# Kernel tuning notes

Hardware: AMD Instinct MI355X
Metric: run time of the kernel (lower is better)

Reference implementation:

```python
import jax, jax.numpy as jnp
import numpy as np

B, M, D, E, K, T = 8192, 6, 128, 5, 2, 60
SHARED_W, UNSHARED_W, LB_W = 0.3, 0.7, 0.01

def _gelu(x):
    return jax.nn.gelu(x, approximate=False)

def _mlp3(x, w1, b1, w2, b2, w3, b3):
    h = _gelu(x @ w1 + b1)
    h = _gelu(h @ w2 + b2)
    return h @ w3 + b3

def _expert_stack(x, w1, b1, w2, b2, w3, b3):
    # x: [N, D]; weights stacked over experts e -> grouped GEMMs
    h = _gelu(jnp.einsum('nd,edh->enh', x, w1) + b1[:, None, :])
    h = _gelu(jnp.einsum('enh,ehg->eng', h, w2) + b2[:, None, :])
    return jnp.einsum('eng,ego->eno', h, w3) + b3[:, None, :]

def setup_inputs():
    key = jax.random.key(0)
    ks = iter(jax.random.split(key, 64))
    p = lambda shape, s=0.05: s * jax.random.normal(next(ks), shape, dtype=jnp.float32)
    return {
        'mode_features': jax.random.normal(next(ks), (B, M, D), dtype=jnp.float32),
        'rw1': p((D, 256)), 'rb1': p((256,)), 'rw2': p((256, 128)), 'rb2': p((128,)),
        'rw3': p((128, E)), 'rb3': p((E,)),
        'sh_tw1': p((D, 256)), 'sh_tb1': p((256,)), 'sh_tw2': p((256, 256)), 'sh_tb2': p((256,)),
        'sh_tw3': p((256, T * 2)), 'sh_tb3': p((T * 2,)),
        'sh_sw1': p((D, 128)), 'sh_sb1': p((128,)), 'sh_sw2': p((128, 64)), 'sh_sb2': p((64,)),
        'sh_sw3': p((64, 1)), 'sh_sb3': p((1,)),
        'ex_tw1': p((E, D, 256)), 'ex_tb1': p((E, 256)), 'ex_tw2': p((E, 256, 256)), 'ex_tb2': p((E, 256)),
        'ex_tw3': p((E, 256, T * 2)), 'ex_tb3': p((E, T * 2)),
        'ex_sw1': p((E, D, 128)), 'ex_sb1': p((E, 128)), 'ex_sw2': p((E, 128, 64)), 'ex_sb2': p((E, 64)),
        'ex_sw3': p((E, 64, 1)), 'ex_sb3': p((E, 1)),
    }

def reference(mode_features, rw1, rb1, rw2, rb2, rw3, rb3,
              sh_tw1, sh_tb1, sh_tw2, sh_tb2, sh_tw3, sh_tb3,
              sh_sw1, sh_sb1, sh_sw2, sh_sb2, sh_sw3, sh_sb3,
              ex_tw1, ex_tb1, ex_tw2, ex_tb2, ex_tw3, ex_tb3,
              ex_sw1, ex_sb1, ex_sw2, ex_sb2, ex_sw3, ex_sb3):
    b, m, d = mode_features.shape
    x = mode_features.reshape(b * m, d)
    # router (Dropout is identity in eval mode)
    logits = _mlp3(x, rw1, rb1, rw2, rb2, rw3, rb3)                 # [N, E]
    probs = jax.nn.softmax(logits, axis=-1)
    router_logits = logits.reshape(b, m, E)
    topk_logits, topk_idx = jax.lax.top_k(router_logits, K)         # [B, M, K]
    topk_probs = jax.nn.softmax(topk_logits, axis=-1)
    # shared expert on all tokens
    shared_traj = _mlp3(x, sh_tw1, sh_tb1, sh_tw2, sh_tb2, sh_tw3, sh_tb3).reshape(b, m, T, 2)
    shared_score = _mlp3(x, sh_sw1, sh_sb1, sh_sw2, sh_sb2, sh_sw3, sh_sb3).reshape(b, m)
    # all unshared experts computed densely (torch code also computes these for expert_predictions)
    traj_all = _expert_stack(x, ex_tw1, ex_tb1, ex_tw2, ex_tb2, ex_tw3, ex_tb3).reshape(E, b, m, T, 2)
    score_all = _expert_stack(x, ex_sw1, ex_sb1, ex_sw2, ex_sb2, ex_sw3, ex_sb3).reshape(E, b, m)
    # top-k combine: gather selected expert outputs (same math as the torch dispatch + index_add_)
    traj_bme = jnp.transpose(traj_all, (1, 2, 0, 3, 4))             # [B, M, E, T, 2]
    score_bme = jnp.transpose(score_all, (1, 2, 0))                 # [B, M, E]
    idx5 = jnp.broadcast_to(topk_idx[..., None, None], (b, m, K, T, 2))
    sel_traj = jnp.take_along_axis(traj_bme, idx5, axis=2)          # [B, M, K, T, 2]
    sel_score = jnp.take_along_axis(score_bme, topk_idx, axis=2)    # [B, M, K]
    unshared_traj = jnp.einsum('bmktc,bmk->bmtc', sel_traj, topk_probs)
    unshared_score = jnp.sum(sel_score * topk_probs, axis=-1)
    final_traj = SHARED_W * shared_traj + UNSHARED_W * unshared_traj
    final_score = SHARED_W * shared_score + UNSHARED_W * unshared_score
    # load-balance aux loss
    avg_probs = jnp.mean(probs, axis=0)                             # [E]
    entropy = -jnp.sum(avg_probs * jnp.log(avg_probs + 1e-8))
    l2 = jnp.mean((avg_probs - 1.0 / E) ** 2)
    aux_loss = -entropy * LB_W + 0.01 * l2
    return (final_traj, final_score, router_logits, topk_idx, aux_loss, traj_all, score_all)
```

## Files before the change

kernel.cpp:

```cpp
#include <hip/hip_runtime.h>
#include <hip/hip_bf16.h>
#include <cstdint>
#include <cstddef>

static constexpr int N_TOK = 49152;
static constexpr size_t OFF_TRAJ     = 0;
static constexpr size_t OFF_SCORE    = 5898240;
static constexpr size_t OFF_LOGITS   = 5947392;
static constexpr size_t OFF_IDX      = 6193152;
static constexpr size_t OFF_AUX      = 6291456;
static constexpr size_t OFF_TRAJALL  = 6291457;
static constexpr size_t OFF_SCOREALL = 35782657;

typedef short s16x8 __attribute__((ext_vector_type(8)));
typedef float f32x4 __attribute__((ext_vector_type(4)));
typedef f32x4 f32x4u __attribute__((aligned(4)));
typedef unsigned int u32;
typedef unsigned short u16;

static constexpr u32 O_T1 = 0,      O_T2 = 196608, O_T3 = 589824;
static constexpr u32 O_S1 = 774144, O_S2 = 872448;
static constexpr u32 OB_T1 = 0, OB_T2 = 1536, OB_T3 = 3072, OB_S1 = 3792, OB_S2 = 4560;
static constexpr u32 OW_S3 = 4944, OB_S3 = 5328;

__device__ __forceinline__ float gelu_exact(float x) {
    return 0.5f * x * (1.0f + erff(x * 0.70710678118654752440f));
}
__device__ __forceinline__ float gelu_f(float x) {
    const float x2 = x * x;
    const float u  = x * fmaf(0.07135486172f, x2, 1.5957691216057308f);
    const float t  = __expf(-u);
    return x * __builtin_amdgcn_rcpf(1.0f + t);
}
__device__ __forceinline__ float bf2f(u16 u) {
    return __uint_as_float(((u32)u) << 16);
}
__device__ __forceinline__ u16 f2bf(float v) {
    return ((__hip_bfloat16_raw)__float2bfloat16(v)).x;
}
__device__ __forceinline__ void gload16(const u16* g, u16* l) {
    __builtin_amdgcn_global_load_lds(
        (const __attribute__((address_space(1))) u32*)g,
        (__attribute__((address_space(3))) u32*)l, 16, 0, 0);
}
#define MFMA16(a, b, c) __builtin_amdgcn_mfma_f32_16x16x32_bf16(a, b, c, 0, 0, 0)
#define SBAR() __builtin_amdgcn_sched_barrier(0)

__device__ __forceinline__ s16x8 lds_frag(const u16* buf, int RBu16, int r, int c) {
    return *(const s16x8*)&buf[r * RBu16 + ((c ^ (r & 7)) << 3)];
}
__device__ __forceinline__ void lds_store4(u16* buf, int RBu16, int r, int colb,
                                           float v0, float v1, float v2, float v3) {
    const int ch = (colb >> 3) ^ (r & 7);
    ushort4 st = { f2bf(v0), f2bf(v1), f2bf(v2), f2bf(v3) };
    *(ushort4*)&buf[r * RBu16 + ch * 8 + (colb & 7)] = st;
}

__global__ __launch_bounds__(512, 2)
void router_fused(const float* __restrict__ x, const float* __restrict__ rw1,
                  const float* __restrict__ rb1, const float* __restrict__ rw2,
                  const float* __restrict__ rb2, const float* __restrict__ rw3,
                  const float* __restrict__ rb3, u16* __restrict__ xb,
                  float* __restrict__ logits, float* __restrict__ oidx,
                  float* __restrict__ tp, int* __restrict__ ti,
                  float* __restrict__ part)
{
    __shared__ float bufA[32 * 128];
    __shared__ float bufB[32 * 256];
    __shared__ float bufC[32 * 256];

    const int tid  = threadIdx.x;
    const int row0 = blockIdx.x * 32;
    const int tg   = tid >> 6;
    const int cl   = tid & 63;
    const int t0   = tg * 4;

    {
        const float* src = x + (size_t)row0 * 128;
        #pragma unroll
        for (int i = 0; i < 2; ++i)
            *(float4*)&bufA[i * 2048 + tid * 4] = *(const float4*)&src[i * 2048 + tid * 4];
    }
    __syncthreads();

    {
        u16* dst = xb + (size_t)row0 * 128;
        const int base = tid * 8;
        ushort4 o0, o1;
        o0.x = f2bf(bufA[base + 0]); o0.y = f2bf(bufA[base + 1]);
        o0.z = f2bf(bufA[base + 2]); o0.w = f2bf(bufA[base + 3]);
        o1.x = f2bf(bufA[base + 4]); o1.y = f2bf(bufA[base + 5]);
        o1.z = f2bf(bufA[base + 6]); o1.w = f2bf(bufA[base + 7]);
        *(ushort4*)&dst[base]     = o0;
        *(ushort4*)&dst[base + 4] = o1;
    }

    float acc1[4][4] = {};
    for (int k0 = 0; k0 < 128; k0 += 32) {
        __syncthreads();
        #pragma unroll
        for (int i = 0; i < 4; ++i)
            *(float4*)&bufB[i * 2048 + tid * 4] =
                *(const float4*)&rw1[(size_t)k0 * 256 + i * 2048 + tid * 4];
        __syncthreads();
        #pragma unroll
        for (int kk = 0; kk < 32; ++kk) {
            const float4 wv = *(const float4*)&bufB[kk * 256 + cl * 4];
            #pragma unroll
            for (int i = 0; i < 4; ++i) {
                const float xv = bufA[(t0 + i) * 128 + k0 + kk];
                acc1[i][0] = fmaf(xv, wv.x, acc1[i][0]);
                acc1[i][1] = fmaf(xv, wv.y, acc1[i][1]);
                acc1[i][2] = fmaf(xv, wv.z, acc1[i][2]);
                acc1[i][3] = fmaf(xv, wv.w, acc1[i][3]);
            }
        }
    }
    {
        const float4 b1 = *(const float4*)&rb1[cl * 4];
        #pragma unroll
        for (int i = 0; i < 4; ++i) {
            bufC[(t0 + i) * 256 + cl * 4 + 0] = gelu_exact(acc1[i][0] + b1.x);
            bufC[(t0 + i) * 256 + cl * 4 + 1] = gelu_exact(acc1[i][1] + b1.y);
            bufC[(t0 + i) * 256 + cl * 4 + 2] = gelu_exact(acc1[i][2] + b1.z);
            bufC[(t0 + i) * 256 + cl * 4 + 3] = gelu_exact(acc1[i][3] + b1.w);
        }
    }
    __syncthreads();

    float acc2[4][2] = {};
    for (int k0 = 0; k0 < 256; k0 += 32) {
        __syncthreads();
        #pragma unroll
        for (int i = 0; i < 2; ++i)
            *(float4*)&bufA[i * 2048 + tid * 4] =
                *(const float4*)&rw2[(size_t)k0 * 128 + i * 2048 + tid * 4];
        __syncthreads();
        #pragma unroll
        for (int kk = 0; kk < 32; ++kk) {
            const float2 wv = *(const float2*)&bufA[kk * 128 + cl * 2];
            #pragma unroll
            for (int i = 0; i < 4; ++i) {
                const float hv = bufC[(t0 + i) * 256 + k0 + kk];
                acc2[i][0] = fmaf(hv, wv.x, acc2[i][0]);
                acc2[i][1] = fmaf(hv, wv.y, acc2[i][1]);
            }
        }
    }
    {
        const float2 b2 = *(const float2*)&rb2[cl * 2];
        #pragma unroll
        for (int i = 0; i < 4; ++i) {
            bufB[(t0 + i) * 128 + cl * 2 + 0] = gelu_exact(acc2[i][0] + b2.x);
            bufB[(t0 + i) * 128 + cl * 2 + 1] = gelu_exact(acc2[i][1] + b2.y);
        }
    }
    __syncthreads();

    {
        const int tok = tid >> 4;
        const int ln  = tid & 15;
        float l5[5] = {0.f, 0.f, 0.f, 0.f, 0.f};
        #pragma unroll
        for (int kk = 0; kk < 8; ++kk) {
            const float hv = bufB[tok * 128 + ln * 8 + kk];
            #pragma unroll
            for (int e = 0; e < 5; ++e)
                l5[e] = fmaf(hv, rw3[(size_t)(ln * 8 + kk) * 5 + e], l5[e]);
        }
        #pragma unroll
        for (int off = 8; off > 0; off >>= 1)
            #pragma unroll
            for (int e = 0; e < 5; ++e)
                l5[e] += __shfl_xor(l5[e], off);

        if (ln == 0) {
            const int n = row0 + tok;
            float l[5];
            #pragma unroll
            for (int e = 0; e < 5; ++e) {
                l[e] = l5[e] + rb3[e];
                logits[(size_t)n * 5 + e] = l[e];
            }
            float m = l[0];
            #pragma unroll
            for (int e = 1; e < 5; ++e) m = fmaxf(m, l[e]);
            float p[5], s = 0.f;
            #pragma unroll
            for (int e = 0; e < 5; ++e) { p[e] = expf(l[e] - m); s += p[e]; }
            const float inv = 1.0f / s;
            #pragma unroll
            for (int e = 0; e < 5; ++e) bufC[tok * 5 + e] = p[e] * inv;

            int i0 = 0; float v0 = l[0];
            #pragma unroll
            for (int e = 1; e < 5; ++e) if (l[e] > v0) { v0 = l[e]; i0 = e; }
            int i1 = -1; float v1 = -1e30f;
            #pragma unroll
            for (int e = 0; e < 5; ++e) if (e != i0 && l[e] > v1) { v1 = l[e]; i1 = e; }

            const float t  = expf(v1 - v0);
            const float q0 = 1.0f / (1.0f + t);
            const float q1 = t / (1.0f + t);

            oidx[(size_t)n * 2]     = (float)i0;
            oidx[(size_t)n * 2 + 1] = (float)i1;
            tp[n * 2] = q0; tp[n * 2 + 1] = q1;
            ti[n * 2] = i0; ti[n * 2 + 1] = i1;
        }
    }
    __syncthreads();
    if (tid < 5) {
        float s = 0.f;
        #pragma unroll 8
        for (int t = 0; t < 32; ++t) s += bufC[t * 5 + tid];
        part[blockIdx.x * 5 + tid] = s;
    }
}

__global__ __launch_bounds__(256)
void aux_kernel(const float* __restrict__ part, float* __restrict__ aux)
{
    __shared__ float avg[5];
    const int tid = threadIdx.x;
    if (tid < 5) {
        float s = 0.f;
        for (int b = 0; b < 1536; ++b) s += part[b * 5 + tid];
        avg[tid] = s / (float)N_TOK;
    }
    __syncthreads();
    if (tid == 0) {
        float ent = 0.f, l2 = 0.f;
        #pragma unroll
        for (int e = 0; e < 5; ++e) {
            ent -= avg[e] * logf(avg[e] + 1e-8f);
            float d = avg[e] - 0.2f;
            l2 += d * d;
        }
        l2 *= (1.0f / 5.0f);
        aux[0] = -ent * 0.01f + 0.01f * l2;
    }
}

__global__ __launch_bounds__(512, 2)
void expert_fused(const u16* __restrict__ xb, const u16* __restrict__ wtb,
                  const float* __restrict__ biasp, float* __restrict__ out,
                  float* __restrict__ shtraj, float* __restrict__ shscore)
{
    __shared__ u16 xs[64 * 128];
    __shared__ u16 hb[64 * 256];
    float* hbf = (float*)hb;
    u16* s1p = hb;
    u16* s2p = hb + 64 * 128;

    const int tid  = threadIdx.x;
    const int lane = tid & 63;
    const int wave = tid >> 6;
    const int row0 = blockIdx.x * 64;
    const int e    = blockIdx.y;
    const int frow = lane & 15;
    const int kgrp = lane >> 4;
    const int c0   = wave * 32;

    #pragma unroll
    for (int i = 0; i < 2; ++i) {
        const int idx = i * 512 + tid;
        const int r = idx >> 4, c = idx & 15;
        gload16(xb + (size_t)(row0 + r) * 128 + ((c ^ (r & 7)) << 3), &xs[idx * 8]);
    }

    const int col3 = wave * 16 + kgrp * 4;
    const int r3   = (wave * 16 + frow) < 120 ? (wave * 16 + frow) : 119;

    s16x8 wf1[4][2];
    {
        const u16* w1p = wtb + O_T1 + e * 32768;
        #pragma unroll
        for (int n = 0; n < 2; ++n) {
            const u16* p = w1p + (size_t)(c0 + n * 16 + frow) * 128 + kgrp * 8;
            #pragma unroll
            for (int ks = 0; ks < 4; ++ks) wf1[ks][n] = *(const s16x8*)(p + ks * 32);
        }
    }
    SBAR();

    __syncthreads();

    f32x4 acc1[4][2] = {};
    #pragma unroll
    for (int ks = 0; ks < 4; ++ks)
        #pragma unroll
        for (int m = 0; m < 4; ++m) {
            const s16x8 a = lds_frag(xs, 128, m * 16 + frow, ks * 4 + kgrp);
            #pragma unroll
            for (int n = 0; n < 2; ++n)
                acc1[m][n] = MFMA16(wf1[ks][n], a, acc1[m][n]);
        }

    const u16* w2p = wtb + O_T2 + e * 65536;
    s16x8 wf2a[4][2];
    f32x4 bb1[2];
    #pragma unroll
    for (int n = 0; n < 2; ++n) {
        const u16* p = w2p + (size_t)(c0 + n * 16 + frow) * 256 + kgrp * 8;
        #pragma unroll
        for (int ks = 0; ks < 4; ++ks) wf2a[ks][n] = *(const s16x8*)(p + ks * 32);
        bb1[n] = *(const f32x4*)&biasp[OB_T1 + e * 256 + c0 + n * 16 + kgrp * 4];
    }
    SBAR();

    {
        #pragma unroll
        for (int n = 0; n < 2; ++n) {
            const int colb = c0 + n * 16 + kgrp * 4;
            #pragma unroll
            for (int m = 0; m < 4; ++m)
                lds_store4(hb, 256, m * 16 + frow, colb,
                           gelu_f(acc1[m][n][0] + bb1[n][0]),
                           gelu_f(acc1[m][n][1] + bb1[n][1]),
                           gelu_f(acc1[m][n][2] + bb1[n][2]),
                           gelu_f(acc1[m][n][3] + bb1[n][3]));
        }
    }
    __syncthreads();

    s16x8 wf2b[4][2];
    #pragma unroll
    for (int n = 0; n < 2; ++n) {
        const u16* p = w2p + (size_t)(c0 + n * 16 + frow) * 256 + 128 + kgrp * 8;
        #pragma unroll
        for (int ks = 0; ks < 4; ++ks) wf2b[ks][n] = *(const s16x8*)(p + ks * 32);
    }
    SBAR();

    f32x4 acc2[4][2] = {};
    #pragma unroll
    for (int ks = 0; ks < 4; ++ks)
        #pragma unroll
        for (int m = 0; m < 4; ++m) {
            const s16x8 a = lds_frag(hb, 256, m * 16 + frow, ks * 4 + kgrp);
            #pragma unroll
            for (int n = 0; n < 2; ++n)
                acc2[m][n] = MFMA16(wf2a[ks][n], a, acc2[m][n]);
        }
    #pragma unroll
    for (int ks = 0; ks < 4; ++ks)
        #pragma unroll
        for (int m = 0; m < 4; ++m) {
            const s16x8 a = lds_frag(hb, 256, m * 16 + frow, (ks + 4) * 4 + kgrp);
            #pragma unroll
            for (int n = 0; n < 2; ++n)
                acc2[m][n] = MFMA16(wf2b[ks][n], a, acc2[m][n]);
        }

    s16x8 wf3[8];
    f32x4 bb2[2];
    {
        const u16* w3p = wtb + O_T3 + e * 30720 + (size_t)r3 * 256 + kgrp * 8;
        #pragma unroll
        for (int ks = 0; ks < 8; ++ks) wf3[ks] = *(const s16x8*)(w3p + ks * 32);
        #pragma unroll
        for (int n = 0; n < 2; ++n)
            bb2[n] = *(const f32x4*)&biasp[OB_T2 + e * 256 + c0 + n * 16 + kgrp * 4];
    }
    SBAR();
    __syncthreads();

    {
        #pragma unroll
        for (int n = 0; n < 2; ++n) {
            const int colb = c0 + n * 16 + kgrp * 4;
            #pragma unroll
            for (int m = 0; m < 4; ++m)
                lds_store4(hb, 256, m * 16 + frow, colb,
                           gelu_f(acc2[m][n][0] + bb2[n][0]),
                           gelu_f(acc2[m][n][1] + bb2[n][1]),
                           gelu_f(acc2[m][n][2] + bb2[n][2]),
                           gelu_f(acc2[m][n][3] + bb2[n][3]));
        }
    }
    __syncthreads();

    s16x8 wfs1[4];
    f32x4 bb3 = *(const f32x4u*)&biasp[OB_T3 + e * 120 + (col3 < 120 ? col3 : 116)];
    {
        const u16* p = wtb + O_S1 + e * 16384 + (size_t)(wave * 16 + frow) * 128 + kgrp * 8;
        #pragma unroll
        for (int ks = 0; ks < 4; ++ks) wfs1[ks] = *(const s16x8*)(p + ks * 32);
    }
    SBAR();

    f32x4 acc3[4] = {};
    #pragma unroll
    for (int ks = 0; ks < 8; ++ks)
        #pragma unroll
        for (int m = 0; m < 4; ++m) {
            const s16x8 a = lds_frag(hb, 256, m * 16 + frow, ks * 4 + kgrp);
            acc3[m] = MFMA16(wf3[ks], a, acc3[m]);
        }
    __syncthreads();

    f32x4 accs1[4] = {};
    #pragma unroll
    for (int ks = 0; ks < 4; ++ks)
        #pragma unroll
        for (int m = 0; m < 4; ++m) {
            const s16x8 a = lds_frag(xs, 128, m * 16 + frow, ks * 4 + kgrp);
            accs1[m] = MFMA16(wfs1[ks], a, accs1[m]);
        }
    s16x8 wfs2[4];
    f32x4 bbs1;
    {
        const u16* p = wtb + O_S2 + e * 8192 + (size_t)((wave & 3) * 16 + frow) * 128 + kgrp * 8;
        #pragma unroll
        for (int ks = 0; ks < 4; ++ks) wfs2[ks] = *(const s16x8*)(p + ks * 32);
        bbs1 = *(const f32x4*)&biasp[OB_S1 + e * 128 + wave * 16 + kgrp * 4];
    }
    SBAR();
    {
        const int colb = wave * 16 + kgrp * 4;
        #pragma unroll
        for (int m = 0; m < 4; ++m)
            lds_store4(s1p, 128, m * 16 + frow, colb,
                       gelu_f(accs1[m][0] + bbs1[0]),
                       gelu_f(accs1[m][1] + bbs1[1]),
                       gelu_f(accs1[m][2] + bbs1[2]),
                       gelu_f(accs1[m][3] + bbs1[3]));
    }
    __syncthreads();

    if (wave < 4) {
        f32x4 accs2[4] = {};
        #pragma unroll
        for (int ks = 0; ks < 4; ++ks)
            #pragma unroll
            for (int m = 0; m < 4; ++m) {
                const s16x8 a = lds_frag(s1p, 128, m * 16 + frow, ks * 4 + kgrp);
                accs2[m] = MFMA16(wfs2[ks], a, accs2[m]);
            }
        const int colb = wave * 16 + kgrp * 4;
        const f32x4 bb = *(const f32x4*)&biasp[OB_S2 + e * 64 + colb];
        #pragma unroll
        for (int m = 0; m < 4; ++m)
            lds_store4(s2p, 64, m * 16 + frow, colb,
                       gelu_f(accs2[m][0] + bb[0]),
                       gelu_f(accs2[m][1] + bb[1]),
                       gelu_f(accs2[m][2] + bb[2]),
                       gelu_f(accs2[m][3] + bb[3]));
    }
    __syncthreads();

    {
        const int tok = tid >> 3;
        const int kc  = tid & 7;
        const float* w3s = biasp + OW_S3 + e * 64 + kc * 8;
        const s16x8 v = lds_frag(s2p, 64, tok, kc);
        float p = 0.f;
        #pragma unroll
        for (int j = 0; j < 8; ++j) p = fmaf(bf2f((u16)v[j]), w3s[j], p);
        p += __shfl_xor(p, 1);
        p += __shfl_xor(p, 2);
        p += __shfl_xor(p, 4);
        if (kc == 0) {
            const float val = p + biasp[OB_S3 + e];
            if (e < 5) out[OFF_SCOREALL + (size_t)e * N_TOK + row0 + tok] = val;
            else       shscore[row0 + tok] = val;
        }
    }
    __syncthreads();

    if (col3 < 120) {
        #pragma unroll
        for (int m = 0; m < 4; ++m) {
            f32x4 v;
            #pragma unroll
            for (int j = 0; j < 4; ++j) v[j] = acc3[m][j] + bb3[j];
            *(f32x4*)&hbf[(m * 16 + frow) * 124 + col3] = v;
        }
    }
    __syncthreads();

    {
        float* dst = (e < 5) ? out + OFF_TRAJALL + ((size_t)e * N_TOK + row0) * 120
                             : shtraj + (size_t)row0 * 120;
        const int head = (int)((16 - (((size_t)dst) & 15)) & 15) >> 2;
        const int nvec = (7680 - head) >> 2;
        const int tail = 7680 - head - (nvec << 2);
        if (tid < head) {
            const int t0i = tid;
            dst[t0i] = hbf[(t0i / 120) * 124 + (t0i % 120)];
        }
        if (tid >= 8 && tid < 8 + tail) {
            const int t0i = 7680 - tail + (tid - 8);
            dst[t0i] = hbf[(t0i / 120) * 124 + (t0i % 120)];
        }
        #pragma unroll
        for (int i = 0; i < 4; ++i) {
            const int v = i * 512 + tid;
            if (v < nvec) {
                const int q = head + v * 4;
                const int tok = q / 120;
                const int colq = q - tok * 120;
                f32x4 val;
                #pragma unroll
                for (int j = 0; j < 4; ++j) {
                    const int qq = q + j;
                    const int tk = qq / 120;
                    val[j] = hbf[tk * 124 + (qq - tk * 120)];
                }
                (void)tok; (void)colq;
                *(f32x4*)(dst + q) = val;
            }
        }
    }
}

__global__ __launch_bounds__(256)
void combine_all(const float* __restrict__ trajall, const float* __restrict__ shtraj,
                 const float* __restrict__ scoreall, const float* __restrict__ shscore,
                 const float* __restrict__ tp, const int* __restrict__ ti,
                 float* __restrict__ ftraj, float* __restrict__ fscore)
{
    const int i4 = blockIdx.x * 256 + threadIdx.x;
    const int n  = i4 / 30;
    const int q4 = (i4 - n * 30) * 4;
    const int i0 = ti[n * 2], i1 = ti[n * 2 + 1];
    const float p0 = tp[n * 2], p1 = tp[n * 2 + 1];

    const f32x4 a = *(const f32x4u*)&trajall[((size_t)i0 * N_TOK + n) * 120 + q4];
    const f32x4 b = *(const f32x4u*)&trajall[((size_t)i1 * N_TOK + n) * 120 + q4];
    const f32x4 s = *(const f32x4*)&shtraj[(size_t)n * 120 + q4];
    f32x4 r;
    #pragma unroll
    for (int j = 0; j < 4; ++j)
        r[j] = 0.3f * s[j] + 0.7f * (p0 * a[j] + p1 * b[j]);
    *(f32x4*)&ftraj[(size_t)n * 120 + q4] = r;

    if (q4 == 0) {
        const float sa = scoreall[(size_t)i0 * N_TOK + n];
        const float sb = scoreall[(size_t)i1 * N_TOK + n];
        fscore[n] = 0.3f * shscore[n] + 0.7f * (p0 * sa + p1 * sb);
    }
}

struct WDesc { const float* src; u32 dstOff; int K, H, nz; };
struct WTable { WDesc d[10]; };

__global__ __launch_bounds__(256)
void convert_w(WTable t, u16* __restrict__ dst)
{
    const WDesc dd = t.d[blockIdx.y];
    const int tilesK = dd.K >> 5;
    const int tilesH = (dd.H + 31) >> 5;
    const int tt = blockIdx.x;
    if (tt >= tilesK * tilesH * dd.nz) return;
    const int e  = tt / (tilesK * tilesH);
    const int r  = tt - e * (tilesK * tilesH);
    const int th = r / tilesK;
    const int tk = r - th * tilesK;

    __shared__ float tile[32][33];
    const int tx = threadIdx.x & 31;
    const int ty = threadIdx.x >> 5;

    #pragma unroll
// ... 32 lines not shown

    const float* x   = (const float*)d_in[0];
    const float* rw1 = (const float*)d_in[1];
    const float* rb1 = (const float*)d_in[2];
    const float* rw2 = (const float*)d_in[3];
    const float* rb2 = (const float*)d_in[4];
    const float* rw3 = (const float*)d_in[5];
    const float* rb3 = (const float*)d_in[6];

    float* out = (float*)d_out;
    char* ws = (char*)d_ws;

    u16*   xb      = (u16*)(ws);
    u16*   wtb     = (u16*)(ws + 12582912);
    float* biasp   = (float*)(ws + 14426112);
    float* part    = (float*)(ws + 14447616);
    float* tp      = (float*)(ws + 14478336);
    int*   ti      = (int*)  (ws + 14871552);
    float* shscore = (float*)(ws + 15264768);
    float* shtraj  = (float*)(ws + 15461376);

    const dim3 blk(256);

    router_fused<<<dim3(N_TOK / 32), dim3(512), 0, stream>>>(
        x, rw1, rb1, rw2, rb2, rw3, rb3, xb,
        out + OFF_LOGITS, out + OFF_IDX, tp, ti, part);
    aux_kernel<<<dim3(1), blk, 0, stream>>>(part, out + OFF_AUX);

    {
        WTable t;
        t.d[0] = { (const float*)d_in[19], O_T1,              128, 256, 5 };
        t.d[1] = { (const float*)d_in[7],  O_T1 + 5 * 32768,  128, 256, 1 };
        t.d[2] = { (const float*)d_in[21], O_T2,              256, 256, 5 };
        t.d[3] = { (const float*)d_in[9],  O_T2 + 5 * 65536,  256, 256, 1 };
        t.d[4] = { (const float*)d_in[23], O_T3,              256, 120, 5 };
        t.d[5] = { (const float*)d_in[11], O_T3 + 5 * 30720,  256, 120, 1 };
        t.d[6] = { (const float*)d_in[25], O_S1,              128, 128, 5 };
        t.d[7] = { (const float*)d_in[13], O_S1 + 5 * 16384,  128, 128, 1 };
        t.d[8] = { (const float*)d_in[27], O_S2,              128,  64, 5 };
        t.d[9] = { (const float*)d_in[15], O_S2 + 5 * 8192,   128,  64, 1 };
        convert_w<<<dim3(320, 10), blk, 0, stream>>>(t, wtb);
    }
    {
        CTable t;
        t.d[0]  = { (const float*)d_in[20], OB_T1,        1280 };
        t.d[1]  = { (const float*)d_in[8],  OB_T1 + 1280,  256 };
        t.d[2]  = { (const float*)d_in[22], OB_T2,        1280 };
        t.d[3]  = { (const float*)d_in[10], OB_T2 + 1280,  256 };
        t.d[4]  = { (const float*)d_in[24], OB_T3,         600 };
        t.d[5]  = { (const float*)d_in[12], OB_T3 + 600,   120 };
        t.d[6]  = { (const float*)d_in[26], OB_S1,         640 };
        t.d[7]  = { (const float*)d_in[14], OB_S1 + 640,   128 };
        t.d[8]  = { (const float*)d_in[28], OB_S2,         320 };
        t.d[9]  = { (const float*)d_in[16], OB_S2 + 320,    64 };
        t.d[10] = { (const float*)d_in[29], OW_S3,         320 };
        t.d[11] = { (const float*)d_in[17], OW_S3 + 320,    64 };
        t.d[12] = { (const float*)d_in[30], OB_S3,           5 };
        t.d[13] = { (const float*)d_in[18], OB_S3 + 5,       1 };
        pack_f32<<<dim3(5, 14), blk, 0, stream>>>(t, biasp);
    }

    expert_fused<<<dim3(N_TOK / 64, 6), dim3(512), 0, stream>>>(
        xb, wtb, biasp, out, shtraj, shscore);

    combine_all<<<dim3(N_TOK * 30 / 256), blk, 0, stream>>>(
        out + OFF_TRAJALL, shtraj, out + OFF_SCOREALL, shscore,
        tp, ti, out + OFF_TRAJ, out + OFF_SCORE);
}
```

Baseline: 416.3 us.

## Merge router and expert kernels into one launch with extra grid rows

The fp32 router MLP and the bf16 MFMA expert MLP now run in one kernel. Grid rows 0-5 do the expert work and rows 6-7 each cover half the router tokens, so the slow SIMT router overlaps with expert work on the GPU instead of running first. The x-to-bf16 conversion moves into a separate small kernel, and the LDS swizzle mask becomes a parameter. The merged kernel shares LDS buffers and launch bounds across both paths, so the router path's occupancy follows the expert path's footprint.

Result: faster. 365.4 us (-12.2%).

```diff
diff --git a/kernel.cpp b/kernel.cpp
--- a/kernel.cpp
+++ b/kernel.cpp
@@ -46,175 +46,434 @@
 #define MFMA16(a, b, c) __builtin_amdgcn_mfma_f32_16x16x32_bf16(a, b, c, 0, 0, 0)
 #define SBAR() __builtin_amdgcn_sched_barrier(0)
 
-__device__ __forceinline__ s16x8 lds_frag(const u16* buf, int RBu16, int r, int c) {
-    return *(const s16x8*)&buf[r * RBu16 + ((c ^ (r & 7)) << 3)];
-}
-__device__ __forceinline__ void lds_store4(u16* buf, int RBu16, int r, int colb,
+__device__ __forceinline__ s16x8 lds_frag(const u16* buf, int RBu16, int r, int c, int mask) {
+    return *(const s16x8*)&buf[r * RBu16 + ((c ^ (r & mask)) << 3)];
+}
+__device__ __forceinline__ void lds_store4(u16* buf, int RBu16, int r, int colb, int mask,
                                            float v0, float v1, float v2, float v3) {
-    const int ch = (colb >> 3) ^ (r & 7);
+    const int ch = (colb >> 3) ^ (r & mask);
     ushort4 st = { f2bf(v0), f2bf(v1), f2bf(v2), f2bf(v3) };
     *(ushort4*)&buf[r * RBu16 + ch * 8 + (colb & 7)] = st;
 }
 
 __global__ __launch_bounds__(512, 2)
-void router_fused(const float* __restrict__ x, const float* __restrict__ rw1,
-                  const float* __restrict__ rb1, const float* __restrict__ rw2,
-                  const float* __restrict__ rb2, const float* __restrict__ rw3,
-                  const float* __restrict__ rb3, u16* __restrict__ xb,
-                  float* __restrict__ logits, float* __restrict__ oidx,
-                  float* __restrict__ tp, int* __restrict__ ti,
-                  float* __restrict__ part)
+void mega_fused(const u16* __restrict__ xb, const u16* __restrict__ wtb,
+                const float* __restrict__ biasp, float* __restrict__ out,
+                float* __restrict__ shtraj, float* __restrict__ shscore,
+                const float* __restrict__ x, const float* __restrict__ rw1,
+                const float* __restrict__ rb1, const float* __restrict__ rw2,
+                const float* __restrict__ rb2, const float* __restrict__ rw3,
+                const float* __restrict__ rb3, float* __restrict__ logits,
+                float* __restrict__ oidx, float* __restrict__ tp,
+                int* __restrict__ ti, float* __restrict__ part)
 {
-    __shared__ float bufA[32 * 128];
-    __shared__ float bufB[32 * 256];
-    __shared__ float bufC[32 * 256];
-
-    const int tid  = threadIdx.x;
-    const int row0 = blockIdx.x * 32;
-    const int tg   = tid >> 6;
-    const int cl   = tid & 63;
-    const int t0   = tg * 4;
-
-    {
-        const float* src = x + (size_t)row0 * 128;
-        #pragma unroll
-        for (int i = 0; i < 2; ++i)
-            *(float4*)&bufA[i * 2048 + tid * 4] = *(const float4*)&src[i * 2048 + tid * 4];
-    }
-    __syncthreads();
-
-    {
-        u16* dst = xb + (size_t)row0 * 128;
-        const int base = tid * 8;
-        ushort4 o0, o1;
-        o0.x = f2bf(bufA[base + 0]); o0.y = f2bf(bufA[base + 1]);
-        o0.z = f2bf(bufA[base + 2]); o0.w = f2bf(bufA[base + 3]);
-        o1.x = f2bf(bufA[base + 4]); o1.y = f2bf(bufA[base + 5]);
-        o1.z = f2bf(bufA[base + 6]); o1.w = f2bf(bufA[base + 7]);
-        *(ushort4*)&dst[base]     = o0;
-        *(ushort4*)&dst[base + 4] = o1;
-    }
-
-    float acc1[4][4] = {};
-    for (int k0 = 0; k0 < 128; k0 += 32) {
+    __shared__ u16 xs[64 * 128];
+    __shared__ u16 hb[64 * 256];
+    float* hbf = (float*)hb;
+    u16* s1p = hb;
+    u16* s2p = hb + 64 * 128;
+
+    const int tid = threadIdx.x;
+    const int ey  = blockIdx.y;
+
+    if (ey >= 6) {
+        float* fA = (float*)xs;
+        float* fB = hbf;
+        const int blk = (ey - 6) * 768 + blockIdx.x;
+        const int r0  = blk * 32;
+        const int tg  = tid >> 6;
+        const int cl  = tid & 63;
+        const int t0  = tg * 4;
+
+        {
+            const float* src = x + (size_t)r0 * 128;
+            #pragma unroll
+            for (int i = 0; i < 2; ++i)
+                *(f32x4*)&fA[i * 2048 + tid * 4] = *(const f32x4*)&src[i * 2048 + tid * 4];
+        }
         __syncthreads();
-        #pragma unroll
-        for (int i = 0; i < 4; ++i)
-            *(float4*)&bufB[i * 2048 + tid * 4] =
-                *(const float4*)&rw1[(size_t)k0 * 256 + i * 2048 + tid * 4];
+
+        float acc1[4][4] = {};
+        for (int k0 = 0; k0 < 128; k0 += 32) {
+            __syncthreads();
+            #pragma unroll
+            for (int i = 0; i < 4; ++i)
+                *(f32x4*)&fB[i * 2048 + tid * 4] =
+                    *(const f32x4*)&rw1[(size_t)k0 * 256 + i * 2048 + tid * 4];
+            __syncthreads();
+            #pragma unroll
+            for (int kk = 0; kk < 32; ++kk) {
+                const f32x4 wv = *(const f32x4*)&fB[kk * 256 + cl * 4];
+                #pragma unroll
+                for (int i = 0; i < 4; ++i) {
+                    const float xv = fA[(t0 + i) * 128 + k0 + kk];
+                    acc1[i][0] = fmaf(xv, wv[0], acc1[i][0]);
+                    acc1[i][1] = fmaf(xv, wv[1], acc1[i][1]);
+                    acc1[i][2] = fmaf(xv, wv[2], acc1[i][2]);
+                    acc1[i][3] = fmaf(xv, wv[3], acc1[i][3]);
+                }
+            }
+        }
         __syncthreads();
-        #pragma unroll
-        for (int kk = 0; kk < 32; ++kk) {
-            const float4 wv = *(const float4*)&bufB[kk * 256 + cl * 4];
+        {
+            const f32x4 b1 = *(const f32x4*)&rb1[cl * 4];
             #pragma unroll
             for (int i = 0; i < 4; ++i) {
-                const float xv = bufA[(t0 + i) * 128 + k0 + kk];
-                acc1[i][0] = fmaf(xv, wv.x, acc1[i][0]);
-                acc1[i][1] = fmaf(xv, wv.y, acc1[i][1]);
-                acc1[i][2] = fmaf(xv, wv.z, acc1[i][2]);
-                acc1[i][3] = fmaf(xv, wv.w, acc1[i][3]);
-            }
-        }
-    }
-    {
-        const float4 b1 = *(const float4*)&rb1[cl * 4];
+                fB[(t0 + i) * 256 + cl * 4 + 0] = gelu_exact(acc1[i][0] + b1[0]);
+                fB[(t0 + i) * 256 + cl * 4 + 1] = gelu_exact(acc1[i][1] + b1[1]);
+                fB[(t0 + i) * 256 + cl * 4 + 2] = gelu_exact(acc1[i][2] + b1[2]);
+                fB[(t0 + i) * 256 + cl * 4 + 3] = gelu_exact(acc1[i][3] + b1[3]);
+            }
+        }
+        __syncthreads();
+
+        float acc2[4][2] = {};
+        for (int k0 = 0; k0 < 256; k0 += 32) {
+            __syncthreads();
+            #pragma unroll
+            for (int i = 0; i < 2; ++i)
+                *(f32x4*)&fA[i * 2048 + tid * 4] =
+                    *(const f32x4*)&rw2[(size_t)k0 * 128 + i * 2048 + tid * 4];
+            __syncthreads();
+            #pragma unroll
+            for (int kk = 0; kk < 32; ++kk) {
+                const float2 wv = *(const float2*)&fA[kk * 128 + cl * 2];
+                #pragma unroll
+                for (int i = 0; i < 4; ++i) {
+                    const float hv = fB[(t0 + i) * 256 + k0 + kk];
+                    acc2[i][0] = fmaf(hv, wv.x, acc2[i][0]);
+                    acc2[i][1] = fmaf(hv, wv.y, acc2[i][1]);
+                }
+            }
+        }
+        __syncthreads();
+        {
+            const float2 b2 = *(const float2*)&rb2[cl * 2];
+            #pragma unroll
+            for (int i = 0; i < 4; ++i) {
+                fA[(t0 + i) * 128 + cl * 2 + 0] = gelu_exact(acc2[i][0] + b2.x);
+                fA[(t0 + i) * 128 + cl * 2 + 1] = gelu_exact(acc2[i][1] + b2.y);
+            }
+        }
+        __syncthreads();
+
+        {
+            const int tok = tid >> 4;
+            const int ln  = tid & 15;
+            float l5[5] = {0.f, 0.f, 0.f, 0.f, 0.f};
+            #pragma unroll
+            for (int kk = 0; kk < 8; ++kk) {
+                const float hv = fA[tok * 128 + ln * 8 + kk];
+                #pragma unroll
+                for (int e = 0; e < 5; ++e)
+                    l5[e] = fmaf(hv, rw3[(size_t)(ln * 8 + kk) * 5 + e], l5[e]);
+            }
+            #pragma unroll
+            for (int off = 8; off > 0; off >>= 1)
+                #pragma unroll
+                for (int e = 0; e < 5; ++e)
+                    l5[e] += __shfl_xor(l5[e], off);
+
+            if (ln == 0) {
+                const int n = r0 + tok;
+                float l[5];
+                #pragma unroll
+                for (int e = 0; e < 5; ++e) {
+                    l[e] = l5[e] + rb3[e];
+                    logits[(size_t)n * 5 + e] = l[e];
+                }
+                float m = l[0];
+                #pragma unroll
+                for (int e = 1; e < 5; ++e) m = fmaxf(m, l[e]);
+                float p[5], s = 0.f;
+                #pragma unroll
+                for (int e = 0; e < 5; ++e) { p[e] = expf(l[e] - m); s += p[e]; }
+                const float inv = 1.0f / s;
+                #pragma unroll
+                for (int e = 0; e < 5; ++e) fB[tok * 5 + e] = p[e] * inv;
+
+                int i0 = 0; float v0 = l[0];
+                #pragma unroll
+                for (int e = 1; e < 5; ++e) if (l[e] > v0) { v0 = l[e]; i0 = e; }
+                int i1 = -1; float v1 = -1e30f;
+                #pragma unroll
+                for (int e = 0; e < 5; ++e) if (e != i0 && l[e] > v1) { v1 = l[e]; i1 = e; }
+
+                const float t  = expf(v1 - v0);
+                const float q0 = 1.0f / (1.0f + t);
+                const float q1 = t / (1.0f + t);
+
+                oidx[(size_t)n * 2]     = (float)i0;
+                oidx[(size_t)n * 2 + 1] = (float)i1;
+                tp[n * 2] = q0; tp[n * 2 + 1] = q1;
+                ti[n * 2] = i0; ti[n * 2 + 1] = i1;
+            }
+        }
+        __syncthreads();
+        if (tid < 5) {
+            float s = 0.f;
+            #pragma unroll 8
+            for (int t = 0; t < 32; ++t) s += fB[t * 5 + tid];
+            part[blk * 5 + tid] = s;
+        }
+        return;
+    }
+
+    const int lane = tid & 63;
+    const int wave = tid >> 6;
+    const int row0 = blockIdx.x * 64;
+    const int e    = ey;
+    const int frow = lane & 15;
+    const int kgrp = lane >> 4;
+    const int c0   = wave * 32;
+
+    #pragma unroll
+    for (int i = 0; i < 2; ++i) {
+        const int idx = i * 512 + tid;
+        const int r = idx >> 4, c = idx & 15;
+        gload16(xb + (size_t)(row0 + r) * 128 + ((c ^ (r & 15)) << 3), &xs[idx * 8]);
+    }
+
+    const int col3 = wave * 16 + kgrp * 4;
+    const int r3   = (wave * 16 + frow) < 120 ? (wave * 16 + frow) : 119;
+
+    s16x8 wf1[4][2];
+    {
+        const u16* w1p = wtb + O_T1 + e * 32768;
+        #pragma unroll
+        for (int n = 0; n < 2; ++n) {
+            const u16* p = w1p + (size_t)(c0 + n * 16 + frow) * 128 + kgrp * 8;
+            #pragma unroll
+            for (int ks = 0; ks < 4; ++ks) wf1[ks][n] = *(const s16x8*)(p + ks * 32);
+        }
+    }
+    SBAR();
+
+    __syncthreads();
+
+    f32x4 acc1[4][2] = {};
+    #pragma unroll
+    for (int ks = 0; ks < 4; ++ks)
+        #pragma unroll
+        for (int m = 0; m < 4; ++m) {
+            const s16x8 a = lds_frag(xs, 128, m * 16 + frow, ks * 4 + kgrp, 15);
+            #pragma unroll
+            for (int n = 0; n < 2; ++n)
+                acc1[m][n] = MFMA16(wf1[ks][n], a, acc1[m][n]);
+        }
+
+    const u16* w2p = wtb + O_T2 + e * 65536;
+    s16x8 wf2a[4][2];
+    f32x4 bb1[2];
+    #pragma unroll
+    for (int n = 0; n < 2; ++n) {
+        const u16* p = w2p + (size_t)(c0 + n * 16 + frow) * 256 + kgrp * 8;
+        #pragma unroll
+        for (int ks = 0; ks < 4; ++ks) wf2a[ks][n] = *(const s16x8*)(p + ks * 32);
+        bb1[n] = *(const f32x4*)&biasp[OB_T1 + e * 256 + c0 + n * 16 + kgrp * 4];
+    }
+    SBAR();
+
+    {
+        #pragma unroll
+        for (int n = 0; n < 2; ++n) {
+            const int colb = c0 + n * 16 + kgrp * 4;
+            #pragma unroll
+            for (int m = 0; m < 4; ++m)
+                lds_store4(hb, 256, m * 16 + frow, colb, 15,
+                           gelu_f(acc1[m][n][0] + bb1[n][0]),
+                           gelu_f(acc1[m][n][1] + bb1[n][1]),
+                           gelu_f(acc1[m][n][2] + bb1[n][2]),
+                           gelu_f(acc1[m][n][3] + bb1[n][3]));
+        }
+    }
+    __syncthreads();
+
+    s16x8 wf2b[4][2];
+    #pragma unroll
+    for (int n = 0; n < 2; ++n) {
+        const u16* p = w2p + (size_t)(c0 + n * 16 + frow) * 256 + 128 + kgrp * 8;
+        #pragma unroll
+        for (int ks = 0; ks < 4; ++ks) wf2b[ks][n] = *(const s16x8*)(p + ks * 32);
+    }
+    SBAR();
+
+    f32x4 acc2[4][2] = {};
+    #pragma unroll
+    for (int ks = 0; ks < 4; ++ks)
+        #pragma unroll
+        for (int m = 0; m < 4; ++m) {
+            const s16x8 a = lds_frag(hb, 256, m * 16 + frow, ks * 4 + kgrp, 15);
+            #pragma unroll
+            for (int n = 0; n < 2; ++n)
+                acc2[m][n] = MFMA16(wf2a[ks][n], a, acc2[m][n]);
+        }
+    #pragma unroll
+    for (int ks = 0; ks < 4; ++ks)
+        #pragma unroll
+        for (int m = 0; m < 4; ++m) {
+            const s16x8 a = lds_frag(hb, 256, m * 16 + frow, (ks + 4) * 4 + kgrp, 15);
+            #pragma unroll
+            for (int n = 0; n < 2; ++n)
+                acc2[m][n] = MFMA16(wf2b[ks][n], a, acc2[m][n]);
+        }
+
+    s16x8 wf3[8];
+    f32x4 bb2[2];
+    {
+        const u16* w3p = wtb + O_T3 + e * 30720 + (size_t)r3 * 256 + kgrp * 8;
+        #pragma unroll
+        for (int ks = 0; ks < 8; ++ks) wf3[ks] = *(const s16x8*)(w3p + ks * 32);
+        #pragma unroll
+        for (int n = 0; n < 2; ++n)
+            bb2[n] = *(const f32x4*)&biasp[OB_T2 + e * 256 + c0 + n * 16 + kgrp * 4];
+    }
+    SBAR();
+    __syncthreads();
+
+    {
+        #pragma unroll
+        for (int n = 0; n < 2; ++n) {
+            const int colb = c0 + n * 16 + kgrp * 4;
+            #pragma unroll
+            for (int m = 0; m < 4; ++m)
+                lds_store4(hb, 256, m * 16 + frow, colb, 15,
+                           gelu_f(acc2[m][n][0] + bb2[n][0]),
+                           gelu_f(acc2[m][n][1] + bb2[n][1]),
+                           gelu_f(acc2[m][n][2] + bb2[n][2]),
+                           gelu_f(acc2[m][n][3] + bb2[n][3]));
+        }
+    }
+    __syncthreads();
+
+    s16x8 wfs1[4];
+    f32x4 bb3 = *(const f32x4u*)&biasp[OB_T3 + e * 120 + (col3 < 120 ? col3 : 116)];
+    {
+        const u16* p = wtb + O_S1 + e * 16384 + (size_t)(wave * 16 + frow) * 128 + kgrp * 8;
+        #pragma unroll
+        for (int ks = 0; ks < 4; ++ks) wfs1[ks] = *(const s16x8*)(p + ks * 32);
+    }
+    SBAR();
+
+    f32x4 acc3[4] = {};
+    #pragma unroll
+    for (int ks = 0; ks < 8; ++ks)
+        #pragma unroll
+        for (int m = 0; m < 4; ++m) {
+            const s16x8 a = lds_frag(hb, 256, m * 16 + frow, ks * 4 + kgrp, 15);
+            acc3[m] = MFMA16(wf3[ks], a, acc3[m]);
+        }
+    __syncthreads();
+
+    f32x4 accs1[4] = {};
+    #pragma unroll
+    for (int ks = 0; ks < 4; ++ks)
+        #pragma unroll
+        for (int m = 0; m < 4; ++m) {
+            const s16x8 a = lds_frag(xs, 128, m * 16 + frow, ks * 4 + kgrp, 15);
+            accs1[m] = MFMA16(wfs1[ks], a, accs1[m]);
+        }
+    s16x8 wfs2[4];
+    f32x4 bbs1;
+    {
+        const u16* p = wtb + O_S2 + e * 8192 + (size_t)((wave & 3) * 16 + frow) * 128 + kgrp * 8;
+        #pragma unroll
+        for (int ks = 0; ks < 4; ++ks) wfs2[ks] = *(const s16x8*)(p + ks * 32);
+        bbs1 = *(const f32x4*)&biasp[OB_S1 + e * 128 + wave * 16 + kgrp * 4];
+    }
+    SBAR();
+    {
+        const int colb = wave * 16 + kgrp * 4;
+        #pragma unroll
+        for (int m = 0; m < 4; ++m)
+            lds_store4(s1p, 128, m * 16 + frow, colb, 15,
+                       gelu_f(accs1[m][0] + bbs1[0]),
+                       gelu_f(accs1[m][1] + bbs1[1]),
+                       gelu_f(accs1[m][2] + bbs1[2]),
+                       gelu_f(accs1[m][3] + bbs1[3]));
+    }
+    __syncthreads();
+
+    if (wave < 4) {
+        f32x4 accs2[4] = {};
+        #pragma unroll
+        for (int ks = 0; ks < 4; ++ks)
+            #pragma unroll
+            for (int m = 0; m < 4; ++m) {
+                const s16x8 a = lds_frag(s1p, 128, m * 16 + frow, ks * 4 + kgrp, 15);
+                accs2[m] = MFMA16(wfs2[ks], a, accs2[m]);
+            }
+        const int colb = wave * 16 + kgrp * 4;
+        const f32x4 bb = *(const f32x4*)&biasp[OB_S2 + e * 64 + colb];
+        #pragma unroll
+        for (int m = 0; m < 4; ++m)
+            lds_store4(s2p, 64, m * 16 + frow, colb, 7,
+                       gelu_f(accs2[m][0] + bb[0]),
+                       gelu_f(accs2[m][1] + bb[1]),
+                       gelu_f(accs2[m][2] + bb[2]),
+                       gelu_f(accs2[m][3] + bb[3]));
+    }
+    __syncthreads();
+
+    {
+        const int tok = tid >> 3;
+        const int kc  = tid & 7;
+        const float* w3s = biasp + OW_S3 + e * 64 + kc * 8;
+        const s16x8 v = lds_frag(s2p, 64, tok, kc, 7);
+        float p = 0.f;
+        #pragma unroll
+        for (int j = 0; j < 8; ++j) p = fmaf(bf2f((u16)v[j]), w3s[j], p);
+        p += __shfl_xor(p, 1);
+        p += __shfl_xor(p, 2);
+        p += __shfl_xor(p, 4);
+        if (kc == 0) {
+            const float val = p + biasp[OB_S3 + e];
+            if (e < 5) out[OFF_SCOREALL + (size_t)e * N_TOK + row0 + tok] = val;
+            else       shscore[row0 + tok] = val;
+        }
+    }
+    __syncthreads();
+
+    if (col3 < 120) {
+        #pragma unroll
+        for (int m = 0; m < 4; ++m) {
+            f32x4 v;
+            #pragma unroll
+            for (int j = 0; j < 4; ++j) v[j] = acc3[m][j] + bb3[j];
+            *(f32x4*)&hbf[(m * 16 + frow) * 124 + col3] = v;
+        }
+    }
+    __syncthreads();
+
+    {
+        float* dst = (e < 5) ? out + OFF_TRAJALL + ((size_t)e * N_TOK + row0) * 120
+                             : shtraj + (size_t)row0 * 120;
+        const int head = (int)((16 - (((size_t)dst) & 15)) & 15) >> 2;
+        const int nvec = (7680 - head) >> 2;
+        const int tail = 7680 - head - (nvec << 2);
+        if (tid < head) {
+            const int t0i = tid;
+            dst[t0i] = hbf[(t0i / 120) * 124 + (t0i % 120)];
+        }
+        if (tid >= 8 && tid < 8 + tail) {
+            const int t0i = 7680 - tail + (tid - 8);
+            dst[t0i] = hbf[(t0i / 120) * 124 + (t0i % 120)];
+        }
         #pragma unroll
         for (int i = 0; i < 4; ++i) {
-            bufC[(t0 + i) * 256 + cl * 4 + 0] = gelu_exact(acc1[i][0] + b1.x);
-            bufC[(t0 + i) * 256 + cl * 4 + 1] = gelu_exact(acc1[i][1] + b1.y);
-            bufC[(t0 + i) * 256 + cl * 4 + 2] = gelu_exact(acc1[i][2] + b1.z);
-            bufC[(t0 + i) * 256 + cl * 4 + 3] = gelu_exact(acc1[i][3] + b1.w);
-        }
-    }
-    __syncthreads();
-
-    float acc2[4][2] = {};
-    for (int k0 = 0; k0 < 256; k0 += 32) {
-        __syncthreads();
-        #pragma unroll
-        for (int i = 0; i < 2; ++i)
-            *(float4*)&bufA[i * 2048 + tid * 4] =
-                *(const float4*)&rw2[(size_t)k0 * 128 + i * 2048 + tid * 4];
-        __syncthreads();
-        #pragma unroll
-        for (int kk = 0; kk < 32; ++kk) {
-            const float2 wv = *(const float2*)&bufA[kk * 128 + cl * 2];
-            #pragma unroll
-            for (int i = 0; i < 4; ++i) {
-                const float hv = bufC[(t0 + i) * 256 + k0 + kk];
-                acc2[i][0] = fmaf(hv, wv.x, acc2[i][0]);
-                acc2[i][1] = fmaf(hv, wv.y, acc2[i][1]);
-            }
-        }
-    }
-    {
-        const float2 b2 = *(const float2*)&rb2[cl * 2];
-        #pragma unroll
-        for (int i = 0; i < 4; ++i) {
-            bufB[(t0 + i) * 128 + cl * 2 + 0] = gelu_exact(acc2[i][0] + b2.x);
-            bufB[(t0 + i) * 128 + cl * 2 + 1] = gelu_exact(acc2[i][1] + b2.y);
-        }
-    }
-    __syncthreads();
-
-    {
-        const int tok = tid >> 4;
-        const int ln  = tid & 15;
-        float l5[5] = {0.f, 0.f, 0.f, 0.f, 0.f};
-        #pragma unroll
-        for (int kk = 0; kk < 8; ++kk) {
-            const float hv = bufB[tok * 128 + ln * 8 + kk];
-            #pragma unroll
-            for (int e = 0; e < 5; ++e)
-                l5[e] = fmaf(hv, rw3[(size_t)(ln * 8 + kk) * 5 + e], l5[e]);
-        }
-        #pragma unroll
-        for (int off = 8; off > 0; off >>= 1)
-            #pragma unroll
-            for (int e = 0; e < 5; ++e)
-                l5[e] += __shfl_xor(l5[e], off);
-
-        if (ln == 0) {
-            const int n = row0 + tok;
-            float l[5];
-            #pragma unroll
-            for (int e = 0; e < 5; ++e) {
-                l[e] = l5[e] + rb3[e];
-                logits[(size_t)n * 5 + e] = l[e];
-            }
-            float m = l[0];
-            #pragma unroll
-            for (int e = 1; e < 5; ++e) m = fmaxf(m, l[e]);
-            float p[5], s = 0.f;
-            #pragma unroll
-            for (int e = 0; e < 5; ++e) { p[e] = expf(l[e] - m); s += p[e]; }
-            const float inv = 1.0f / s;
-            #pragma unroll
-            for (int e = 0; e < 5; ++e) bufC[tok * 5 + e] = p[e] * inv;
-
-            int i0 = 0; float v0 = l[0];
-            #pragma unroll
-            for (int e = 1; e < 5; ++e) if (l[e] > v0) { v0 = l[e]; i0 = e; }
-            int i1 = -1; float v1 = -1e30f;
-            #pragma unroll
-            for (int e = 0; e < 5; ++e) if (e != i0 && l[e] > v1) { v1 = l[e]; i1 = e; }
-
-            const float t  = expf(v1 - v0);
-            const float q0 = 1.0f / (1.0f + t);
-            const float q1 = t / (1.0f + t);
-
-            oidx[(size_t)n * 2]     = (float)i0;
-            oidx[(size_t)n * 2 + 1] = (float)i1;
-            tp[n * 2] = q0; tp[n * 2 + 1] = q1;
-            ti[n * 2] = i0; ti[n * 2 + 1] = i1;
-        }
-    }
-    __syncthreads();
-    if (tid < 5) {
-        float s = 0.f;
-        #pragma unroll 8
-        for (int t = 0; t < 32; ++t) s += bufC[t * 5 + tid];
-        part[blockIdx.x * 5 + tid] = s;
+            const int v = i * 512 + tid;
+            if (v < nvec) {
+                const int q = head + v * 4;
+                f32x4 val;
+                #pragma unroll
+                for (int j = 0; j < 4; ++j) {
+                    const int qq = q + j;
+                    const int tk = qq / 120;
+                    val[j] = hbf[tk * 124 + (qq - tk * 120)];
+                }
+                *(f32x4*)(dst + q) = val;
+            }
+        }
     }
 }
 
@@ -239,279 +498,6 @@
         }
         l2 *= (1.0f / 5.0f);
         aux[0] = -ent * 0.01f + 0.01f * l2;
-    }
-}
-
-__global__ __launch_bounds__(512, 2)
-void expert_fused(const u16* __restrict__ xb, const u16* __restrict__ wtb,
-                  const float* __restrict__ biasp, float* __restrict__ out,
-                  float* __restrict__ shtraj, float* __restrict__ shscore)
-{
-    __shared__ u16 xs[64 * 128];
-    __shared__ u16 hb[64 * 256];
-    float* hbf = (float*)hb;
-    u16* s1p = hb;
-    u16* s2p = hb + 64 * 128;
-
-    const int tid  = threadIdx.x;
-    const int lane = tid & 63;
-    const int wave = tid >> 6;
-    const int row0 = blockIdx.x * 64;
-    const int e    = blockIdx.y;
-    const int frow = lane & 15;
-    const int kgrp = lane >> 4;
-    const int c0   = wave * 32;
-
-    #pragma unroll
-    for (int i = 0; i < 2; ++i) {
-        const int idx = i * 512 + tid;
-        const int r = idx >> 4, c = idx & 15;
-        gload16(xb + (size_t)(row0 + r) * 128 + ((c ^ (r & 7)) << 3), &xs[idx * 8]);
-    }
-
-    const int col3 = wave * 16 + kgrp * 4;
-    const int r3   = (wave * 16 + frow) < 120 ? (wave * 16 + frow) : 119;
-
-    s16x8 wf1[4][2];
-    {
-        const u16* w1p = wtb + O_T1 + e * 32768;
-        #pragma unroll
-        for (int n = 0; n < 2; ++n) {
-            const u16* p = w1p + (size_t)(c0 + n * 16 + frow) * 128 + kgrp * 8;
-            #pragma unroll
-            for (int ks = 0; ks < 4; ++ks) wf1[ks][n] = *(const s16x8*)(p + ks * 32);
-        }
-    }
-    SBAR();
-
-    __syncthreads();
-
-    f32x4 acc1[4][2] = {};
-    #pragma unroll
-    for (int ks = 0; ks < 4; ++ks)
-        #pragma unroll
-        for (int m = 0; m < 4; ++m) {
-            const s16x8 a = lds_frag(xs, 128, m * 16 + frow, ks * 4 + kgrp);
-            #pragma unroll
-            for (int n = 0; n < 2; ++n)
-                acc1[m][n] = MFMA16(wf1[ks][n], a, acc1[m][n]);
-        }
-
-    const u16* w2p = wtb + O_T2 + e * 65536;
-    s16x8 wf2a[4][2];
-    f32x4 bb1[2];
-    #pragma unroll
-    for (int n = 0; n < 2; ++n) {
-        const u16* p = w2p + (size_t)(c0 + n * 16 + frow) * 256 + kgrp * 8;
-        #pragma unroll
-        for (int ks = 0; ks < 4; ++ks) wf2a[ks][n] = *(const s16x8*)(p + ks * 32);
-        bb1[n] = *(const f32x4*)&biasp[OB_T1 + e * 256 + c0 + n * 16 + kgrp * 4];
-    }
-    SBAR();
-
-    {
-        #pragma unroll
-        for (int n = 0; n < 2; ++n) {
-            const int colb = c0 + n * 16 + kgrp * 4;
-            #pragma unroll
-            for (int m = 0; m < 4; ++m)
-                lds_store4(hb, 256, m * 16 + frow, colb,
-                           gelu_f(acc1[m][n][0] + bb1[n][0]),
-                           gelu_f(acc1[m][n][1] + bb1[n][1]),
-                           gelu_f(acc1[m][n][2] + bb1[n][2]),
-                           gelu_f(acc1[m][n][3] + bb1[n][3]));
-        }
-    }
-    __syncthreads();
-
-    s16x8 wf2b[4][2];
-    #pragma unroll
-    for (int n = 0; n < 2; ++n) {
-        const u16* p = w2p + (size_t)(c0 + n * 16 + frow) * 256 + 128 + kgrp * 8;
-        #pragma unroll
-        for (int ks = 0; ks < 4; ++ks) wf2b[ks][n] = *(const s16x8*)(p + ks * 32);
-    }
-    SBAR();
-
-    f32x4 acc2[4][2] = {};
-    #pragma unroll
-    for (int ks = 0; ks < 4; ++ks)
-        #pragma unroll
-        for (int m = 0; m < 4; ++m) {
-            const s16x8 a = lds_frag(hb, 256, m * 16 + frow, ks * 4 + kgrp);
-            #pragma unroll
-            for (int n = 0; n < 2; ++n)
-                acc2[m][n] = MFMA16(wf2a[ks][n], a, acc2[m][n]);
-        }
-    #pragma unroll
-    for (int ks = 0; ks < 4; ++ks)
-        #pragma unroll
-        for (int m = 0; m < 4; ++m) {
-            const s16x8 a = lds_frag(hb, 256, m * 16 + frow, (ks + 4) * 4 + kgrp);
-            #pragma unroll
-            for (int n = 0; n < 2; ++n)
-                acc2[m][n] = MFMA16(wf2b[ks][n], a, acc2[m][n]);
-        }
-
-    s16x8 wf3[8];
-    f32x4 bb2[2];
-    {
-        const u16* w3p = wtb + O_T3 + e * 30720 + (size_t)r3 * 256 + kgrp * 8;
-        #pragma unroll
-        for (int ks = 0; ks < 8; ++ks) wf3[ks] = *(const s16x8*)(w3p + ks * 32);
-        #pragma unroll
-        for (int n = 0; n < 2; ++n)
-            bb2[n] = *(const f32x4*)&biasp[OB_T2 + e * 256 + c0 + n * 16 + kgrp * 4];
-    }
-    SBAR();
-    __syncthreads();
-
-    {
-        #pragma unroll
-        for (int n = 0; n < 2; ++n) {
-            const int colb = c0 + n * 16 + kgrp * 4;
-            #pragma unroll
-            for (int m = 0; m < 4; ++m)
-                lds_store4(hb, 256, m * 16 + frow, colb,
-                           gelu_f(acc2[m][n][0] + bb2[n][0]),
-                           gelu_f(acc2[m][n][1] + bb2[n][1]),
-                           gelu_f(acc2[m][n][2] + bb2[n][2]),
-                           gelu_f(acc2[m][n][3] + bb2[n][3]));
-        }
-    }
-    __syncthreads();
-
-    s16x8 wfs1[4];
-    f32x4 bb3 = *(const f32x4u*)&biasp[OB_T3 + e * 120 + (col3 < 120 ? col3 : 116)];
-    {
-        const u16* p = wtb + O_S1 + e * 16384 + (size_t)(wave * 16 + frow) * 128 + kgrp * 8;
-        #pragma unroll
-        for (int ks = 0; ks < 4; ++ks) wfs1[ks] = *(const s16x8*)(p + ks * 32);
-    }
-    SBAR();
-
-    f32x4 acc3[4] = {};
-    #pragma unroll
-    for (int ks = 0; ks < 8; ++ks)
-        #pragma unroll
-        for (int m = 0; m < 4; ++m) {
-            const s16x8 a = lds_frag(hb, 256, m * 16 + frow, ks * 4 + kgrp);
-            acc3[m] = MFMA16(wf3[ks], a, acc3[m]);
-        }
-    __syncthreads();
-
-    f32x4 accs1[4] = {};
-    #pragma unroll
-    for (int ks = 0; ks < 4; ++ks)
-        #pragma unroll
-        for (int m = 0; m < 4; ++m) {
-            const s16x8 a = lds_frag(xs, 128, m * 16 + frow, ks * 4 + kgrp);
-            accs1[m] = MFMA16(wfs1[ks], a, accs1[m]);
-        }
-    s16x8 wfs2[4];
-    f32x4 bbs1;
-    {
-        const u16* p = wtb + O_S2 + e * 8192 + (size_t)((wave & 3) * 16 + frow) * 128 + kgrp * 8;
-        #pragma unroll
-        for (int ks = 0; ks < 4; ++ks) wfs2[ks] = *(const s16x8*)(p + ks * 32);
-        bbs1 = *(const f32x4*)&biasp[OB_S1 + e * 128 + wave * 16 + kgrp * 4];
-    }
-    SBAR();
-    {
-        const int colb = wave * 16 + kgrp * 4;
-        #pragma unroll
-        for (int m = 0; m < 4; ++m)
-            lds_store4(s1p, 128, m * 16 + frow, colb,
-                       gelu_f(accs1[m][0] + bbs1[0]),
-                       gelu_f(accs1[m][1] + bbs1[1]),
-                       gelu_f(accs1[m][2] + bbs1[2]),
-                       gelu_f(accs1[m][3] + bbs1[3]));
-    }
-    __syncthreads();
-
-    if (wave < 4) {
-        f32x4 accs2[4] = {};
-        #pragma unroll
-        for (int ks = 0; ks < 4; ++ks)
-            #pragma unroll
-            for (int m = 0; m < 4; ++m) {
-                const s16x8 a = lds_frag(s1p, 128, m * 16 + frow, ks * 4 + kgrp);
-                accs2[m] = MFMA16(wfs2[ks], a, accs2[m]);
-            }
-        const int colb = wave * 16 + kgrp * 4;
-        const f32x4 bb = *(const f32x4*)&biasp[OB_S2 + e * 64 + colb];
-        #pragma unroll
-        for (int m = 0; m < 4; ++m)
-            lds_store4(s2p, 64, m * 16 + frow, colb,
-                       gelu_f(accs2[m][0] + bb[0]),
-                       gelu_f(accs2[m][1] + bb[1]),
-                       gelu_f(accs2[m][2] + bb[2]),
-                       gelu_f(accs2[m][3] + bb[3]));
-    }
-    __syncthreads();
-
-    {
-        const int tok = tid >> 3;
-        const int kc  = tid & 7;
-        const float* w3s = biasp + OW_S3 + e * 64 + kc * 8;
-        const s16x8 v = lds_frag(s2p, 64, tok, kc);
-        float p = 0.f;
-        #pragma unroll
-        for (int j = 0; j < 8; ++j) p = fmaf(bf2f((u16)v[j]), w3s[j], p);
-        p += __shfl_xor(p, 1);
-        p += __shfl_xor(p, 2);
-        p += __shfl_xor(p, 4);
-        if (kc == 0) {
-            const float val = p + biasp[OB_S3 + e];
-            if (e < 5) out[OFF_SCOREALL + (size_t)e * N_TOK + row0 + tok] = val;
-            else       shscore[row0 + tok] = val;
-        }
-    }
-    __syncthreads();
-
-    if (col3 < 120) {
-        #pragma unroll
-        for (int m = 0; m < 4; ++m) {
-            f32x4 v;
-            #pragma unroll
-            for (int j = 0; j < 4; ++j) v[j] = acc3[m][j] + bb3[j];
-            *(f32x4*)&hbf[(m * 16 + frow) * 124 + col3] = v;
-        }
-    }
-    __syncthreads();
-
-    {
-        float* dst = (e < 5) ? out + OFF_TRAJALL + ((size_t)e * N_TOK + row0) * 120
-                             : shtraj + (size_t)row0 * 120;
-        const int head = (int)((16 - (((size_t)dst) & 15)) & 15) >> 2;
-        const int nvec = (7680 - head) >> 2;
-        const int tail = 7680 - head - (nvec << 2);
-        if (tid < head) {
-            const int t0i = tid;
-            dst[t0i] = hbf[(t0i / 120) * 124 + (t0i % 120)];
-        }
-        if (tid >= 8 && tid < 8 + tail) {
-            const int t0i = 7680 - tail + (tid - 8);
-            dst[t0i] = hbf[(t0i / 120) * 124 + (t0i % 120)];
-        }
-        #pragma unroll
-        for (int i = 0; i < 4; ++i) {
-            const int v = i * 512 + tid;
-            if (v < nvec) {
-                const int q = head + v * 4;
-                const int tok = q / 120;
-                const int colq = q - tok * 120;
-                f32x4 val;
-                #pragma unroll
-                for (int j = 0; j < 4; ++j) {
-                    const int qq = q + j;
-                    const int tk = qq / 120;
-                    val[j] = hbf[tk * 124 + (qq - tk * 120)];
-                }
-                (void)tok; (void)colq;
-                *(f32x4*)(dst + q) = val;
-            }
-        }
     }
 }
 
@@ -541,6 +527,16 @@
         const float sb = scoreall[(size_t)i1 * N_TOK + n];
         fscore[n] = 0.3f * shscore[n] + 0.7f * (p0 * sa + p1 * sb);
     }
+}
+
+__global__ __launch_bounds__(256)
+void convert_x(const float* __restrict__ x, u16* __restrict__ xb)
+{
+    const size_t i = ((size_t)blockIdx.x * 256 + threadIdx.x) * 4;
+    float4 v = *(const float4*)(x + i);
+    ushort4 o;
+    o.x = f2bf(v.x); o.y = f2bf(v.y); o.z = f2bf(v.z); o.w = f2bf(v.w);
+    *(ushort4*)(xb + i) = o;
 }
 
 struct WDesc { const float* src; u32 dstOff; int K, H, nz; };
@@ -619,11 +615,7 @@
 
     const dim3 blk(256);
 
-    router_fused<<<dim3(N_TOK / 32), dim3(512), 0, stream>>>(
-        x, rw1, rb1, rw2, rb2, rw3, rb3, xb,
-        out + OFF_LOGITS, out + OFF_IDX, tp, ti, part);
-    aux_kernel<<<dim3(1), blk, 0, stream>>>(part, out + OFF_AUX);
-
+    convert_x<<<dim3(N_TOK * 128 / 1024), blk, 0, stream>>>(x, xb);
     {
         WTable t;
         t.d[0] = { (const float*)d_in[19], O_T1,              128, 256, 5 };
@@ -657,9 +649,12 @@
         pack_f32<<<dim3(5, 14), blk, 0, stream>>>(t, biasp);
     }
 
-    expert_fused<<<dim3(N_TOK / 64, 6), dim3(512), 0, stream>>>(
-        xb, wtb, biasp, out, shtraj, shscore);
-
+    mega_fused<<<dim3(N_TOK / 64, 8), dim3(512), 0, stream>>>(
+        xb, wtb, biasp, out, shtraj, shscore,
+        x, rw1, rb1, rw2, rb2, rw3, rb3,
+        out + OFF_LOGITS, out + OFF_IDX, tp, ti, part);
+
+    aux_kernel<<<dim3(1), blk, 0, stream>>>(part, out + OFF_AUX);
     combine_all<<<dim3(N_TOK * 30 / 256), blk, 0, stream>>>(
         out + OFF_TRAJALL, shtraj, out + OFF_SCOREALL, shscore,
         tp, ti, out + OFF_TRAJ, out + OFF_SCORE);
```
